# Performance work log

Measured on AMD Instinct MI355X. Metric: run time of the kernel, lower is better.

Reference implementation:

```python
import math
import jax, jax.numpy as jnp
import numpy as np

WS = (8, 7, 7)   # window_size (d, h, w)
SS = (4, 3, 3)   # shift_size
NH = 4           # num_heads
DIM = 128


def _rel_position_index(ws):
    # [N*N] int index into the (2wd-1)(2wh-1)(2ww-1) bias table
    cd, ch, cw = np.arange(ws[0]), np.arange(ws[1]), np.arange(ws[2])
    coords = np.stack(np.meshgrid(cd, ch, cw, indexing='ij')).reshape(3, -1)  # [3, N]
    rel = (coords[:, :, None] - coords[:, None, :]).transpose(1, 2, 0)        # [N, N, 3]
    rel[..., 0] += ws[0] - 1
    rel[..., 1] += ws[1] - 1
    rel[..., 2] += ws[2] - 1
    rel[..., 0] *= (2 * ws[1] - 1) * (2 * ws[2] - 1)
    rel[..., 1] *= (2 * ws[2] - 1)
    return rel.sum(-1).reshape(-1)


def _rel_coords_table(ws):
    # [(2wd-1)(2wh-1)(2ww-1), 3] log-spaced continuous coords (Swin v2)
    rd = np.arange(-(ws[0] - 1), ws[0], dtype=np.float32)
    rh = np.arange(-(ws[1] - 1), ws[1], dtype=np.float32)
    rw = np.arange(-(ws[2] - 1), ws[2], dtype=np.float32)
    t = np.stack(np.meshgrid(rd, rh, rw, indexing='ij')).transpose(1, 2, 3, 0)  # [Td,Th,Tw,3]
    t[..., 0] /= ws[0] - 1
    t[..., 1] /= ws[1] - 1
    t[..., 2] /= ws[2] - 1
    t *= 8.0
    t = np.sign(t) * np.log2(np.abs(t) + 1.0) / 3.0
    return t.reshape(-1, 3)


_REL_INDEX = _rel_position_index(WS)
_COORDS = jnp.asarray(_rel_coords_table(WS))


def _attn_mask(pD, pH, pW, ws, ss):
    img = np.zeros((pD, pH, pW), np.float32)
    sl = lambda w, s: (slice(0, -w), slice(-w, -s), slice(-s, None))
    cnt = 0
    for d in sl(ws[0], ss[0]):
        for h in sl(ws[1], ss[1]):
            for w in sl(ws[2], ss[2]):
                img[d, h, w] = cnt
                cnt += 1
    m = img.reshape(pD // ws[0], ws[0], pH // ws[1], ws[1], pW // ws[2], ws[2])
    m = m.transpose(0, 2, 4, 1, 3, 5).reshape(-1, ws[0] * ws[1] * ws[2])  # [nWin, N]
    diff = m[:, None, :] - m[:, :, None]
    return jnp.asarray(np.where(diff != 0, -100.0, 0.0).astype(np.float32))


def setup_inputs() -> dict:
    key = jax.random.key(0)
    ks = jax.random.split(key, 6)
    B, D, H, W, C = 1, 16, 56, 56, DIM
    g = lambda k, shp, sc: jax.random.normal(k, shp, dtype=jnp.float32) * sc
    return {
        'x': g(ks[0], (B, D, H, W, C), 1.0),
        'qkv_weight': g(ks[1], (3 * C, C), 0.02),
        'qkv_bias': jnp.zeros((3 * C,), jnp.float32),
        'proj_weight': g(ks[2], (C, C), 0.02),
        'proj_bias': jnp.zeros((C,), jnp.float32),
        'logit_scale': jnp.full((NH, 1, 1), float(np.log(10.0)), jnp.float32),
        'cpb_w1': g(ks[3], (512, 3), 0.02),
        'cpb_b1': jnp.zeros((512,), jnp.float32),
        'cpb_w2': g(ks[4], (NH, 512), 0.02),
    }


def reference(x, qkv_weight, qkv_bias, proj_weight, proj_bias,
              logit_scale, cpb_w1, cpb_b1, cpb_w2):
    B, D, H, W, C = x.shape
    wd, wh, ww = WS
    hd = C // NH
    pad_d, pad_h, pad_w = (-D) % wd, (-H) % wh, (-W) % ww
    x = jnp.pad(x, ((0, 0), (0, pad_d), (0, pad_h), (0, pad_w), (0, 0)))
    pD, pH, pW = D + pad_d, H + pad_h, W + pad_w
    ss = [0 if WS[i] >= (pD, pH, pW)[i] else SS[i] for i in range(3)]
    shifted = sum(ss) > 0
    if shifted:
        x = jnp.roll(x, (-ss[0], -ss[1], -ss[2]), axis=(1, 2, 3))
    nd, nh, nw = pD // wd, pH // wh, pW // ww
    nWin, N = nd * nh * nw, wd * wh * ww
    # window partition -> [B*nWin, N, C]
    xw = x.reshape(B, nd, wd, nh, wh, nw, ww, C).transpose(0, 1, 3, 5, 2, 4, 6, 7)
    xw = xw.reshape(B * nWin, N, C)
    # qkv with k-bias zeroed (Swin v2 cosine attention)
    qb = qkv_bias.at[C:2 * C].set(0.0)
    qkv = (xw @ qkv_weight.T + qb).reshape(B * nWin, N, 3, NH, hd).transpose(2, 0, 3, 1, 4)
    q, k, v = qkv[0], qkv[1], qkv[2]   # each [B*nWin, NH, N, hd]
    qn = q / jnp.maximum(jnp.linalg.norm(q, axis=-1, keepdims=True), 1e-12)
    kn = k / jnp.maximum(jnp.linalg.norm(k, axis=-1, keepdims=True), 1e-12)
    attn = jnp.einsum('bhnd,bhmd->bhnm', qn, kn)
    scale = jnp.exp(jnp.minimum(logit_scale, math.log(100.0)))  # [NH,1,1]
    attn = attn * scale
    # continuous relative position bias
    table = jax.nn.relu(_COORDS @ cpb_w1.T + cpb_b1) @ cpb_w2.T  # [T, NH]
    bias = table[_REL_INDEX].reshape(N, N, NH).transpose(2, 0, 1)
    bias = 16.0 * jax.nn.sigmoid(bias)
    attn = attn + bias[None]
    if shifted:
        mask = _attn_mask(pD, pH, pW, WS, ss)  # [nWin, N, N]
        attn = attn.reshape(B, nWin, NH, N, N) + mask[None, :, None]
        attn = attn.reshape(B * nWin, NH, N, N)
    attn = jax.nn.softmax(attn, axis=-1)
    out = jnp.einsum('bhnm,bhmd->bhnd', attn, v).transpose(0, 2, 1, 3).reshape(B * nWin, N, C)
    out = out @ proj_weight.T + proj_bias
    # window reverse -> [B, pD, pH, pW, C]
    out = out.reshape(B, nd, nh, nw, wd, wh, ww, C).transpose(0, 1, 4, 2, 5, 3, 6, 7)
    out = out.reshape(B, pD, pH, pW, C)
    if shifted:
        out = jnp.roll(out, tuple(ss), axis=(1, 2, 3))
    return out[:, :D, :H, :W, :]
```

## Files before the change

### kernel.cpp

```cpp
#include <hip/hip_runtime.h>
#include <hip/hip_bf16.h>

typedef unsigned short u16;
typedef unsigned int   u32;
typedef float f32x4  __attribute__((ext_vector_type(4)));
typedef short bf16x8 __attribute__((ext_vector_type(8)));

#define DI __device__ __forceinline__

constexpr int TBL  = 2535;
constexpr int NTOK = 50176;
constexpr float L2E = 1.4426950408889634f;

constexpr int WB_QW = 0;
constexpr int WB_PW = 49152;
constexpr int WB_QB = 65536;
constexpr int WB_PB = 65920;
constexpr int WB_TOT = 66048;

DI float b2f(u16 u){ return __uint_as_float(((u32)u)<<16); }
DI u16 f2b(float f){
  u32 u = __float_as_uint(f);
  return (u16)((u + 0x7fffu + ((u>>16)&1u)) >> 16);
}
DI float ldf(const void* p, int i, int isf32){
  return isf32 ? ((const float*)p)[i] : b2f(((const u16*)p)[i]);
}
DI f32x4 mfma16(bf16x8 a, bf16x8 b, f32x4 c){
  return __builtin_amdgcn_mfma_f32_16x16x32_bf16(a, b, c, 0, 0, 0);
}
DI u32 cvtpk(float lo, float hi){
  u32 r;
  asm("v_cvt_pk_bf16_f32 %0, %1, %2" : "=v"(r) : "v"(lo), "v"(hi));
  return r;
}
DI float vexp2(float x){
  float r;
  asm("v_exp_f32 %0, %1" : "=v"(r) : "v"(x));
  return r;
}
DI int detect_f32(const void* x, int lane){
  u32 w = ((const u32*)x)[lane];
  u16 lo = (u16)w;
  u32 e = (lo >> 7) & 0xFF;
  int wild = (lo != 0 && (e >= 143 || e <= 111)) ? 1 : 0;
  unsigned long long m = __ballot(wild);
  return __popcll(m) > 16;
}

__global__ void k_cpb(const void* __restrict__ w1, const void* __restrict__ b1,
                      const void* __restrict__ w2, const void* __restrict__ x,
                      const void* __restrict__ qw, const void* __restrict__ pw,
                      const void* __restrict__ qb, const void* __restrict__ pb,
                      u16* __restrict__ wb, float* __restrict__ table16){
  const int lane = threadIdx.x;
  const int isf32 = detect_f32(x, lane);
  {
    int gid = blockIdx.x*64 + lane;
    if (gid < WB_TOT){
      const void* src; int off;
      if (gid < WB_PW)      { src = qw; off = gid; }
      else if (gid < WB_QB) { src = pw; off = gid - WB_PW; }
      else if (gid < WB_PB) { src = qb; off = gid - WB_QB; }
      else                  { src = pb; off = gid - WB_PB; }
      wb[gid] = isf32 ? f2b(((const float*)src)[off]) : ((const u16*)src)[off];
    }
  }
  int t = blockIdx.x;
  int i = t/169; int r = t - i*169; int j = r/13; int k = r - j*13;
  float v0 = 8.f*(float)(i-7)/7.f, v1 = 8.f*(float)(j-6)/6.f, v2 = 8.f*(float)(k-6)/6.f;
  float c0 = copysignf(log2f(fabsf(v0)+1.f)*(1.f/3.f), v0);
  float c1 = copysignf(log2f(fabsf(v1)+1.f)*(1.f/3.f), v1);
  float c2 = copysignf(log2f(fabsf(v2)+1.f)*(1.f/3.f), v2);
  float a0=0.f,a1=0.f,a2=0.f,a3=0.f;
  for (int hh = lane; hh < 512; hh += 64){
    float a = c0*ldf(w1,hh*3,isf32) + c1*ldf(w1,hh*3+1,isf32)
            + c2*ldf(w1,hh*3+2,isf32) + ldf(b1,hh,isf32);
    a = fmaxf(a, 0.f);
    a0 += a*ldf(w2,hh,isf32);       a1 += a*ldf(w2,512+hh,isf32);
    a2 += a*ldf(w2,1024+hh,isf32);  a3 += a*ldf(w2,1536+hh,isf32);
  }
  #pragma unroll
  for (int off=32; off; off>>=1){
    a0 += __shfl_xor(a0, off); a1 += __shfl_xor(a1, off);
    a2 += __shfl_xor(a2, off); a3 += __shfl_xor(a3, off);
  }
  if (lane==0){
    table16[t]       = (16.f/(1.f+__expf(-a0)) - 15.f)*L2E;
    table16[TBL+t]   = (16.f/(1.f+__expf(-a1)) - 15.f)*L2E;
    table16[2*TBL+t] = (16.f/(1.f+__expf(-a2)) - 15.f)*L2E;
    table16[3*TBL+t] = (16.f/(1.f+__expf(-a3)) - 15.f)*L2E;
  }
}

__global__ void k_bias(const float* __restrict__ table16, float* __restrict__ bias16){
  int n = blockIdx.x, h = blockIdx.y;
  int td = n/49; int r2 = n - td*49; int th = r2/7; int tw = r2 - th*7;
  const float* tb = table16 + h*TBL;
  float* o = bias16 + ((size_t)h*392 + n)*392;
  for (int m = threadIdx.x; m < 392; m += 128){
    int sd = m/49; int q2 = m - sd*49; int sh = q2/7; int sw = q2 - sh*7;
    int idx = (td - sd + 7)*169 + (th - sh + 6)*13 + (tw - sw + 6);
    o[m] = tb[idx];
  }
}

__global__ __launch_bounds__(256,3) void k_qkv(const void* __restrict__ x,
    const u16* __restrict__ wb, const void* __restrict__ lsc,
    u16* __restrict__ qkvbuf){
  __shared__ __align__(16) u16 As[64*136];
  __shared__ __align__(16) u16 Ws[128*136];
  const int tid = threadIdx.x;
  const int lane = tid & 63;
  const int isf32 = detect_f32(x, lane);
  const int tokbase0 = blockIdx.x*64;
  {
    int trow = tid>>2, cq = (tid&3)*32;
    int gtok = tokbase0 + trow;
    int win = gtok/392, tt = gtok - win*392;
    int dwi = win>>6, hwi = (win>>3)&7, wwi = win&7;
    int td = tt/49; int r2 = tt - td*49; int th = r2/7; int tw = r2 - th*7;
    int pd = dwi*8 + td + 4; if (pd >= 16) pd -= 16;
    int ph = hwi*7 + th + 3; if (ph >= 56) ph -= 56;
    int pw = wwi*7 + tw + 3; if (pw >= 56) pw -= 56;
    size_t pos = (size_t)((pd*56 + ph)*56 + pw)*128 + cq;
    if (isf32){
      const float4* src = (const float4*)((const float*)x + pos);
      #pragma unroll
      for (int u=0; u<8; ++u){
        float4 a = src[u];
        ushort4 s4 = make_ushort4(f2b(a.x), f2b(a.y), f2b(a.z), f2b(a.w));
        *(ushort4*)&As[trow*136 + cq + u*4] = s4;
      }
    } else {
      const uint4* src = (const uint4*)((const u16*)x + pos);
      #pragma unroll
      for (int u=0; u<4; ++u) *(uint4*)&As[trow*136 + cq + u*8] = src[u];
    }
  }
  const int wave = tid>>6;
  const int c = lane & 15, g = lane >> 4;
  const int tokbase = tokbase0 + wave*16;
  float sl2e[4];
  #pragma unroll
  for (int h2=0; h2<4; ++h2){
    float ls = ldf(lsc, h2, isf32);
    sl2e[h2] = __expf(fminf(ls, 4.60517019f)) * L2E;
  }
  bf16x8 ka[4];
  for (int which = 0; which < 3; ++which){
    __syncthreads();
    {
      int orow = tid>>1, c2 = (tid&1)*64;
      const uint4* src = (const uint4*)(wb + WB_QW + (size_t)(which*128 + orow)*128 + c2);
      #pragma unroll
      for (int u=0; u<8; ++u) *(uint4*)&Ws[orow*136 + c2 + u*8] = src[u];
    }
    __syncthreads();
    if (which == 0){
      #pragma unroll
      for (int kk=0; kk<4; ++kk)
        ka[kk] = *(const bf16x8*)&As[(wave*16 + c)*136 + kk*32 + g*8];
    }
    f32x4 acc[8];
    #pragma unroll
    for (int nt=0; nt<8; ++nt) acc[nt] = 0.f;
    #pragma unroll
    for (int nt=0; nt<8; ++nt){
      #pragma unroll
      for (int kk=0; kk<4; ++kk){
        bf16x8 wf = *(const bf16x8*)&Ws[(nt*16 + c)*136 + kk*32 + g*8];
        acc[nt] = mfma16(ka[kk], wf, acc[nt]);
      }
    }
    if (which != 1){
      #pragma unroll
      for (int nt=0; nt<8; ++nt){
        float bv = b2f(wb[WB_QB + which*128 + nt*16 + c]);
        #pragma unroll
        for (int r=0;r<4;++r) acc[nt][r] += bv;
      }
    }
    if (which < 2){
      #pragma unroll
      for (int h2=0; h2<4; ++h2){
        f32x4 ss;
        #pragma unroll
        for (int r=0;r<4;++r)
          ss[r] = acc[2*h2][r]*acc[2*h2][r] + acc[2*h2+1][r]*acc[2*h2+1][r];
        #pragma unroll
        for (int off=1; off<16; off<<=1){
          #pragma unroll
          for (int r=0;r<4;++r) ss[r] += __shfl_xor(ss[r], off);
        }
        #pragma unroll
        for (int r=0;r<4;++r){
          float rn = rsqrtf(fmaxf(ss[r], 1e-24f));
          if (which == 0) rn *= sl2e[h2];
          acc[2*h2][r]   *= rn;
          acc[2*h2+1][r] *= rn;
        }
      }
    }
    #pragma unroll
    for (int nt=0; nt<8; ++nt){
      int oc = nt*16 + c;
      int head = oc >> 5, chb = oc & 31;
      #pragma unroll
      for (int r=0;r<4;++r){
        int t = tokbase + 4*g + r;
        qkvbuf[((size_t)(which*4+head)*NTOK + t)*32 + chb] = f2b(acc[nt][r]);
      }
    }
  }
}

#define QKT_PAIR(JT, JJ, TAIL) do { \
  bf16x8 kf = *(const bf16x8*)&klds[((JT)*16 + c)*40 + g*8]; \
  f32x4 tz = {0.f,0.f,0.f,0.f}; \
  f32x4 ta = mfma16(kf, qfa, tz); \
  f32x4 tb = mfma16(kf, qfb, tz); \
  const int mb = (JT)*16 + 4*g; \
  const int mbc = (TAIL) ? ((mb <= 388) ? mb : 388) : mb; \
  const float4 ba = *(const float4*)(browA + mbc); \
  const float4 bb = *(const float4*)(browB + mbc); \
  float pa0 = vexp2(ta[0] + ba.x), pa1 = vexp2(ta[1] + ba.y); \
  float pa2 = vexp2(ta[2] + ba.z), pa3 = vexp2(ta[3] + ba.w); \
  float pb0 = vexp2(tb[0] + bb.x), pb1 = vexp2(tb[1] + bb.y); \
  float pb2 = vexp2(tb[2] + bb.z), pb3 = vexp2(tb[3] + bb.w); \
  if (MIXED){ \
    const int4 cm = *(const int4*)&cnt[mbc]; \
    if (cm.x != cnA) pa0 = 0.f;  if (cm.y != cnA) pa1 = 0.f; \
    if (cm.z != cnA) pa2 = 0.f;  if (cm.w != cnA) pa3 = 0.f; \
    if (cm.x != cnB) pb0 = 0.f;  if (cm.y != cnB) pb1 = 0.f; \
    if (cm.z != cnB) pb2 = 0.f;  if (cm.w != cnB) pb3 = 0.f; \
  } \
  if (TAIL && mb > 388){ pa0=0.f; pa1=0.f; pa2=0.f; pa3=0.f; \
                         pb0=0.f; pb1=0.f; pb2=0.f; pb3=0.f; } \
  uint2 wva, wvb; \
  wva.x = cvtpk(pa0,pa1); wva.y = cvtpk(pa2,pa3); \
  wvb.x = cvtpk(pb0,pb1); wvb.y = cvtpk(pb2,pb3); \
  *(uint2*)&psA[c*20 + (JJ)*8 + 2*g] = wva; \
  *(uint2*)&psB[c*20 + (JJ)*8 + 2*g] = wvb; \
} while(0)

#define PV_PAIR(MC) do { \
  bf16x8 pfa = *(const bf16x8*)&psA[c*20 + 4*g]; \
  bf16x8 pfb = *(const bf16x8*)&psB[c*20 + 4*g]; \
  bf16x8 va = *(const bf16x8*)&vT[c*424 + (MC)*32 + g*8]; \
  bf16x8 vb = *(const bf16x8*)&vT[(16+c)*424 + (MC)*32 + g*8]; \
  o0a = mfma16(va, pfa, o0a); o1a = mfma16(vb, pfa, o1a); o2a = mfma16(ones, pfa, o2a); \
  o0b = mfma16(va, pfb, o0b); o1b = mfma16(vb, pfb, o1b); o2b = mfma16(ones, pfb, o2b); \
} while(0)

template<bool MIXED>
DI void attn_main(const u16* __restrict__ qg, const float* __restrict__ bias_h,
                  const u16* klds, const u16* vT, u32* psA, u32* psB, const int* cnt,
                  u16* __restrict__ aout, int win, int h, int wave, int lane){
  const int c = lane & 15, g = lane >> 4;
  const short ob = 0x3F80;
  const bf16x8 ones = {ob,ob,ob,ob,ob,ob,ob,ob};
  for (int pp = wave; pp < 13; pp += 8){
    const int rta = 2*pp;
    const int rtb = (pp < 12) ? (2*pp+1) : 24;
    const bool hasB = (pp < 12);
    const int nbA = rta*16, nbB = rtb*16;
    const int ncA = (nbA + c < 392) ? (nbA + c) : 391;
    const int ncB = (nbB + c < 392) ? (nbB + c) : 391;
    const bf16x8 qfa = *(const bf16x8*)(qg + (size_t)ncA*32 + g*8);
    const bf16x8 qfb = *(const bf16x8*)(qg + (size_t)ncB*32 + g*8);
    const int cnA = MIXED ? cnt[ncA] : 0;
    const int cnB = MIXED ? cnt[ncB] : 0;
    const float* browA = bias_h + (size_t)ncA*392;
    const float* browB = bias_h + (size_t)ncB*392;
    f32x4 o0a = {0.f,0.f,0.f,0.f}, o1a = o0a, o2a = o0a;
    f32x4 o0b = o0a, o1b = o0a, o2b = o0a;
    for (int mc = 0; mc < 12; ++mc){
      QKT_PAIR(2*mc,   0, false);
      QKT_PAIR(2*mc+1, 1, false);
      PV_PAIR(mc);
    }
    QKT_PAIR(24, 0, true);
    { uint2 zz; zz.x = 0u; zz.y = 0u;
      *(uint2*)&psA[c*20 + 8 + 2*g] = zz;
      *(uint2*)&psB[c*20 + 8 + 2*g] = zz; }
    PV_PAIR(12);
    const float rva = 1.f / o2a[0];
    const float rvb = 1.f / o2b[0];
    uint2 wa, wb2;
    wa.x  = cvtpk(o0a[0]*rva, o0a[1]*rva);  wa.y  = cvtpk(o0a[2]*rva, o0a[3]*rva);
    wb2.x = cvtpk(o1a[0]*rva, o1a[1]*rva);  wb2.y = cvtpk(o1a[2]*rva, o1a[3]*rva);
    *(uint2*)&psA[c*20 + 2*g]     = wa;
    *(uint2*)&psA[c*20 + 8 + 2*g] = wb2;
    wa.x  = cvtpk(o0b[0]*rvb, o0b[1]*rvb);  wa.y  = cvtpk(o0b[2]*rvb, o0b[3]*rvb);
    wb2.x = cvtpk(o1b[0]*rvb, o1b[1]*rvb);  wb2.y = cvtpk(o1b[2]*rvb, o1b[3]*rvb);
    *(uint2*)&psB[c*20 + 2*g]     = wa;
    *(uint2*)&psB[c*20 + 8 + 2*g] = wb2;
    const int orow = lane>>2, oq = lane&3;
    uint4 ova = *(const uint4*)&psA[orow*20 + 4*oq];
    const int nA = nbA + orow;
    if (nA < 392)
      *(uint4*)(aout + ((size_t)(win*392 + nA))*128 + h*32 + oq*8) = ova;
    if (hasB){
      uint4 ovb = *(const uint4*)&psB[orow*20 + 4*oq];
      const int nB = nbB + orow;
      if (nB < 392)
        *(uint4*)(aout + ((size_t)(win*392 + nB))*128 + h*32 + oq*8) = ovb;
    }
  }
}

__global__ __launch_bounds__(512,4) void k_attn(const u16* __restrict__ qkv,
    const float* __restrict__ bias16, u16* __restrict__ aout){
  __shared__ __align__(16) u16 klds[400*40];
  __shared__ __align__(16) u16 vT[32*424];
  __shared__ __align__(16) u32 ps[8][640];
  __shared__ __align__(16) int cnt[400];
  const int tid = threadIdx.x;
  const int win = blockIdx.x, h = blockIdx.y;
  const int dwi = win>>6, hwi = (win>>3)&7, wwi = win&7;
  const u16* qg = qkv + ((size_t)(0*4 + h)*NTOK + (size_t)win*392)*32;
  const u16* kg = qkv + ((size_t)(1*4 + h)*NTOK + (size_t)win*392)*32;
  const u16* vg = qkv + ((size_t)(2*4 + h)*NTOK + (size_t)win*392)*32;
  for (int idx = tid; idx < 1600; idx += 512){
    const int row = idx>>2, q = idx&3;
    uint4 a = {0,0,0,0};
    if (row < 392) a = *(const uint4*)(kg + (size_t)row*32 + q*8);
    *(uint4*)&klds[row*40 + q*8] = a;
  }
  for (int idx = tid; idx < 784; idx += 512){
    const int mg = idx>>3, cg = idx&7;
    uint2 v0 = *(const uint2*)(vg + (size_t)(4*mg+0)*32 + cg*4);
    uint2 v1 = *(const uint2*)(vg + (size_t)(4*mg+1)*32 + cg*4);
    uint2 v2 = *(const uint2*)(vg + (size_t)(4*mg+2)*32 + cg*4);
    uint2 v3 = *(const uint2*)(vg + (size_t)(4*mg+3)*32 + cg*4);
    u16 e0[4], e1[4], e2[4], e3[4];
    e0[0]=(u16)v0.x; e0[1]=(u16)(v0.x>>16); e0[2]=(u16)v0.y; e0[3]=(u16)(v0.y>>16);
    e1[0]=(u16)v1.x; e1[1]=(u16)(v1.x>>16); e1[2]=(u16)v1.y; e1[3]=(u16)(v1.y>>16);
    e2[0]=(u16)v2.x; e2[1]=(u16)(v2.x>>16); e2[2]=(u16)v2.y; e2[3]=(u16)(v2.y>>16);
    e3[0]=(u16)v3.x; e3[1]=(u16)(v3.x>>16); e3[2]=(u16)v3.y; e3[3]=(u16)(v3.y>>16);
    #pragma unroll
    for (int cc=0; cc<4; ++cc){
      ushort4 w = make_ushort4(e0[cc], e1[cc], e2[cc], e3[cc]);
      *(ushort4*)&vT[(cg*4+cc)*424 + 4*mg] = w;
    }
  }
  for (int idx = tid; idx < 1024; idx += 512){
    int ch = idx>>5, mm = 392 + (idx&31);
    vT[ch*424 + mm] = 0;
  }
  for (int t2 = tid; t2 < 400; t2 += 512){
    int row = (t2 < 392) ? t2 : 391;
    int td = row/49; int r2 = row - td*49; int th = r2/7; int tw = r2 - th*7;
    int gd = dwi*8 + td, gh = hwi*7 + th, gw = wwi*7 + tw;
    int rd = (gd < 8) ? 0 : ((gd < 12) ? 1 : 2);
    int rh = (gh < 49) ? 0 : ((gh < 53) ? 1 : 2);
    int rw = (gw < 49) ? 0 : ((gw < 53) ? 1 : 2);
    cnt[t2] = rd*9 + rh*3 + rw;
  }
  __syncthreads();
  const int wave = tid>>6, lane = tid&63;
  u32* psA = &ps[wave][0];
  u32* psB = &ps[wave][320];
  const float* bias_h = bias16 + (size_t)h*153664;
  const bool uniform = (dwi == 0) && (hwi < 7) && (wwi < 7);
  if (uniform)
    attn_main<false>(qg, bias_h, klds, vT, psA, psB, cnt, aout, win, h, wave, lane);
  else
    attn_main<true >(qg, bias_h, klds, vT, psA, psB, cnt, aout, win, h, wave, lane);
}

__global__ __launch_bounds__(256,2) void k_proj(const u16* __restrict__ ain,
    const u16* __restrict__ wb, const void* __restrict__ x, void* __restrict__ out){
  __shared__ __align__(16) u16 As[64*136];
  __shared__ __align__(16) u16 Ws[128*136];
  const int tid = threadIdx.x;
  const int lane = tid & 63;
  const int isf32 = detect_f32(x, lane);
  const int tokbase0 = blockIdx.x*64;
  {
    int trow = tid>>2, cq = (tid&3)*32;
    const uint4* src = (const uint4*)(ain + (size_t)(tokbase0+trow)*128 + cq);
    #pragma unroll
    for (int u=0; u<4; ++u) *(uint4*)&As[trow*136 + cq + u*8] = src[u];
  }
  {
    int orow = tid>>1, c2 = (tid&1)*64;
    const uint4* src = (const uint4*)(wb + WB_PW + (size_t)orow*128 + c2);
    #pragma unroll
    for (int u=0; u<8; ++u) *(uint4*)&Ws[orow*136 + c2 + u*8] = src[u];
  }
  __syncthreads();
  const int wave = tid>>6;
  const int c = lane & 15, g = lane >> 4;
  bf16x8 ka[4];
  #pragma unroll
  for (int kk=0; kk<4; ++kk)
    ka[kk] = *(const bf16x8*)&As[(wave*16 + c)*136 + kk*32 + g*8];
  f32x4 acc[8];
  #pragma unroll
  for (int nt=0; nt<8; ++nt) acc[nt] = 0.f;
  #pragma unroll
  for (int nt=0; nt<8; ++nt){
    #pragma unroll
    for (int kk=0; kk<4; ++kk){
      bf16x8 wf = *(const bf16x8*)&Ws[(nt*16 + c)*136 + kk*32 + g*8];
      acc[nt] = mfma16(ka[kk], wf, acc[nt]);
    }
  }
  if (isf32){
    __syncthreads();
    float* WsF = (float*)Ws;
    #pragma unroll
    for (int nt=0; nt<8; ++nt){
      float bv = b2f(wb[WB_PB + nt*16 + c]);
      #pragma unroll
      for (int r=0;r<4;++r)
        WsF[(wave*16 + 4*g + r)*128 + nt*16 + c] = acc[nt][r] + bv;
    }
    __syncthreads();
    const int tok = tid>>2, q4 = tid&3;
    int gtok = tokbase0 + tok;
    int win = gtok/392, tt = gtok - win*392;
    int dwi = win>>6, hwi = (win>>3)&7, wwi = win&7;
    int td = tt/49; int r2 = tt - td*49; int th = r2/7; int tw = r2 - th*7;
    int pd = dwi*8 + td + 4; if (pd >= 16) pd -= 16;
    int ph = hwi*7 + th + 3; if (ph >= 56) ph -= 56;
    int pwx = wwi*7 + tw + 3; if (pwx >= 56) pwx -= 56;
    size_t po = (size_t)((pd*56 + ph)*56 + pwx)*128;
    const float4* srcv = (const float4*)&WsF[tok*128 + q4*32];
    float4* dst = (float4*)((float*)out + po + q4*32);
    #pragma unroll
    for (int i=0;i<8;++i) dst[i] = srcv[i];
  } else {
    const int tokbase = tokbase0 + wave*16;
    size_t po[4];
    #pragma unroll
    for (int r=0;r<4;++r){
      int gtok = tokbase + 4*g + r;
      int win = gtok/392, tt = gtok - win*392;
      int dwi = win>>6, hwi = (win>>3)&7, wwi = win&7;
      int td = tt/49; int r2 = tt - td*49; int th = r2/7; int tw = r2 - th*7;
      int pd = dwi*8 + td + 4; if (pd >= 16) pd -= 16;
      int ph = hwi*7 + th + 3; if (ph >= 56) ph -= 56;
      int pwx = wwi*7 + tw + 3; if (pwx >= 56) pwx -= 56;
      po[r] = (size_t)((pd*56 + ph)*56 + pwx)*128;
    }
    #pragma unroll
    for (int nt=0; nt<8; ++nt){
      int oc = nt*16 + c;
      float bv = b2f(wb[WB_PB + oc]);
      #pragma unroll
      for (int r=0;r<4;++r)
        ((u16*)out)[po[r] + oc] = f2b(acc[nt][r] + bv);
    }
  }
}

extern "C" void kernel_launch(void* const* d_in, const int* in_sizes, int n_in,
                              void* d_out, int out_size, void* d_ws, size_t ws_size,
                              hipStream_t stream){
  const void* x      = d_in[0];
  const void* qkv_w  = d_in[1];
  const void* qkv_b  = d_in[2];
  const void* proj_w = d_in[3];
  const void* proj_b = d_in[4];
  const void* lsc    = d_in[5];
  const void* cpb_w1 = d_in[6];
  const void* cpb_b1 = d_in[7];
  const void* cpb_w2 = d_in[8];
  char* ws = (char*)d_ws;
  float* table16 = (float*)(ws);
  float* bias16  = (float*)(ws + 40960);
  u16*   wb      = (u16*)(ws + 2499584);
  u16*   qkvbuf  = (u16*)(ws + 2631680);
  u16*   attnout = (u16*)(ws + 41166848);

  k_cpb <<<TBL, 64, 0, stream>>>(cpb_w1, cpb_b1, cpb_w2, x,
                                 qkv_w, proj_w, qkv_b, proj_b, wb, table16);
  k_bias<<<dim3(392,4), 128, 0, stream>>>(table16, bias16);
  k_qkv <<<784, 256, 0, stream>>>(x, wb, lsc, qkvbuf);
  k_attn<<<dim3(128,4), 512, 0, stream>>>(qkvbuf, bias16, attnout);
  k_proj<<<784, 256, 0, stream>>>(attnout, wb, x, d_out);
}
```

Measured before the change: 101.7 us.

## Stage QKV output through LDS for coalesced stores; software-prefetch K/bias in attention

The QKV projection kernel now writes its per-lane bf16 results into the shared A tile and then stores each token's 32-channel head segment to global memory as contiguous 16-byte vectors, replacing scattered 2-byte stores. In the attention main loop, the K fragment, bias row and mask-count loads for the next key tile are issued one step ahead, before the current tile's MFMA/exp work, to hide LDS/global latency. This adds extra __syncthreads and register pressure from the double-buffered operands.

Result: slower. 105.5 us (+3.7%).

```diff
diff --git a/kernel.cpp b/kernel.cpp
--- a/kernel.cpp
+++ b/kernel.cpp
@@ -140,7 +140,6 @@
   }
   const int wave = tid>>6;
   const int c = lane & 15, g = lane >> 4;
-  const int tokbase = tokbase0 + wave*16;
   float sl2e[4];
   #pragma unroll
   for (int h2=0; h2<4; ++h2){
@@ -202,41 +201,56 @@
         }
       }
     }
+    __syncthreads();
     #pragma unroll
     for (int nt=0; nt<8; ++nt){
-      int oc = nt*16 + c;
-      int head = oc >> 5, chb = oc & 31;
-      #pragma unroll
-      for (int r=0;r<4;++r){
-        int t = tokbase + 4*g + r;
-        qkvbuf[((size_t)(which*4+head)*NTOK + t)*32 + chb] = f2b(acc[nt][r]);
-      }
-    }
-  }
-}
-
-#define QKT_PAIR(JT, JJ, TAIL) do { \
-  bf16x8 kf = *(const bf16x8*)&klds[((JT)*16 + c)*40 + g*8]; \
+      #pragma unroll
+      for (int r=0;r<4;++r)
+        As[(wave*16 + 4*g + r)*136 + nt*16 + c] = f2b(acc[nt][r]);
+    }
+    __syncthreads();
+    {
+      const int tokl = tid>>2, seg = tid&3;
+      u16* dst = qkvbuf + ((size_t)(which*4+seg)*NTOK + tokbase0 + tokl)*32;
+      const u16* srcl = &As[tokl*136 + seg*32];
+      #pragma unroll
+      for (int u=0; u<4; ++u)
+        *(uint4*)(dst + u*8) = *(const uint4*)(srcl + u*8);
+    }
+  }
+}
+
+DI bf16x8 ldK(const u16* klds, int jt, int c, int g){
+  return *(const bf16x8*)&klds[(jt*16 + c)*40 + g*8];
+}
+DI float4 ldB(const float* brow, int jt, int g){
+  int mbc = jt*16 + 4*g; if (mbc > 388) mbc = 388;
+  return *(const float4*)(brow + mbc);
+}
+DI int4 ldC(const int* cnt, int jt, int g){
+  int mbc = jt*16 + 4*g; if (mbc > 388) mbc = 388;
+  return *(const int4*)&cnt[mbc];
+}
+
+#define QKT_BODY(JJ, TAIL, KF, BA, BB, CM, JT) do { \
   f32x4 tz = {0.f,0.f,0.f,0.f}; \
-  f32x4 ta = mfma16(kf, qfa, tz); \
-  f32x4 tb = mfma16(kf, qfb, tz); \
-  const int mb = (JT)*16 + 4*g; \
-  const int mbc = (TAIL) ? ((mb <= 388) ? mb : 388) : mb; \
-  const float4 ba = *(const float4*)(browA + mbc); \
-  const float4 bb = *(const float4*)(browB + mbc); \
-  float pa0 = vexp2(ta[0] + ba.x), pa1 = vexp2(ta[1] + ba.y); \
-  float pa2 = vexp2(ta[2] + ba.z), pa3 = vexp2(ta[3] + ba.w); \
-  float pb0 = vexp2(tb[0] + bb.x), pb1 = vexp2(tb[1] + bb.y); \
-  float pb2 = vexp2(tb[2] + bb.z), pb3 = vexp2(tb[3] + bb.w); \
+  f32x4 ta = mfma16(KF, qfa, tz); \
+  f32x4 tb = mfma16(KF, qfb, tz); \
+  float pa0 = vexp2(ta[0] + BA.x), pa1 = vexp2(ta[1] + BA.y); \
+  float pa2 = vexp2(ta[2] + BA.z), pa3 = vexp2(ta[3] + BA.w); \
+  float pb0 = vexp2(tb[0] + BB.x), pb1 = vexp2(tb[1] + BB.y); \
+  float pb2 = vexp2(tb[2] + BB.z), pb3 = vexp2(tb[3] + BB.w); \
   if (MIXED){ \
-    const int4 cm = *(const int4*)&cnt[mbc]; \
-    if (cm.x != cnA) pa0 = 0.f;  if (cm.y != cnA) pa1 = 0.f; \
-    if (cm.z != cnA) pa2 = 0.f;  if (cm.w != cnA) pa3 = 0.f; \
-    if (cm.x != cnB) pb0 = 0.f;  if (cm.y != cnB) pb1 = 0.f; \
-    if (cm.z != cnB) pb2 = 0.f;  if (cm.w != cnB) pb3 = 0.f; \
+    if (CM.x != cnA) pa0 = 0.f;  if (CM.y != cnA) pa1 = 0.f; \
+    if (CM.z != cnA) pa2 = 0.f;  if (CM.w != cnA) pa3 = 0.f; \
+    if (CM.x != cnB) pb0 = 0.f;  if (CM.y != cnB) pb1 = 0.f; \
+    if (CM.z != cnB) pb2 = 0.f;  if (CM.w != cnB) pb3 = 0.f; \
   } \
-  if (TAIL && mb > 388){ pa0=0.f; pa1=0.f; pa2=0.f; pa3=0.f; \
-                         pb0=0.f; pb1=0.f; pb2=0.f; pb3=0.f; } \
+  if (TAIL){ \
+    const int mb = (JT)*16 + 4*g; \
+    if (mb > 388){ pa0=0.f; pa1=0.f; pa2=0.f; pa3=0.f; \
+                   pb0=0.f; pb1=0.f; pb2=0.f; pb3=0.f; } \
+  } \
   uint2 wva, wvb; \
   wva.x = cvtpk(pa0,pa1); wva.y = cvtpk(pa2,pa3); \
   wvb.x = cvtpk(pb0,pb1); wvb.y = cvtpk(pb2,pb3); \
@@ -260,6 +274,7 @@
   const int c = lane & 15, g = lane >> 4;
   const short ob = 0x3F80;
   const bf16x8 ones = {ob,ob,ob,ob,ob,ob,ob,ob};
+  const int4 zc = {0,0,0,0};
   for (int pp = wave; pp < 13; pp += 8){
     const int rta = 2*pp;
     const int rtb = (pp < 12) ? (2*pp+1) : 24;
@@ -275,12 +290,22 @@
     const float* browB = bias_h + (size_t)ncB*392;
     f32x4 o0a = {0.f,0.f,0.f,0.f}, o1a = o0a, o2a = o0a;
     f32x4 o0b = o0a, o1b = o0a, o2b = o0a;
+    bf16x8 kf0 = ldK(klds, 0, c, g);
+    float4 ba0 = ldB(browA, 0, g), bb0 = ldB(browB, 0, g);
+    int4   cm0 = MIXED ? ldC(cnt, 0, g) : zc;
     for (int mc = 0; mc < 12; ++mc){
-      QKT_PAIR(2*mc,   0, false);
-      QKT_PAIR(2*mc+1, 1, false);
+      const int jt1 = 2*mc + 1, jt2 = 2*mc + 2;
+      bf16x8 kf1 = ldK(klds, jt1, c, g);
+      float4 ba1 = ldB(browA, jt1, g), bb1 = ldB(browB, jt1, g);
+      int4   cm1 = MIXED ? ldC(cnt, jt1, g) : zc;
+      QKT_BODY(0, false, kf0, ba0, bb0, cm0, 2*mc);
+      kf0 = ldK(klds, jt2, c, g);
+      ba0 = ldB(browA, jt2, g); bb0 = ldB(browB, jt2, g);
+      cm0 = MIXED ? ldC(cnt, jt2, g) : zc;
+      QKT_BODY(1, false, kf1, ba1, bb1, cm1, jt1);
       PV_PAIR(mc);
     }
-    QKT_PAIR(24, 0, true);
+    QKT_BODY(0, true, kf0, ba0, bb0, cm0, 24);
     { uint2 zz; zz.x = 0u; zz.y = 0u;
       *(uint2*)&psA[c*20 + 8 + 2*g] = zz;
       *(uint2*)&psB[c*20 + 8 + 2*g] = zz; }
```
